# Performance work log

Hardware: AMD Instinct MI355X
Metric: run time of the kernel (lower is better)

## Reference

```python
import jax, jax.numpy as jnp
import numpy as np

HEAD_SIZE = 32


def setup_inputs() -> dict:
    key = jax.random.key(0)
    ks = jax.random.split(key, 9)
    B, N, M = 2, 512, 512
    Dq = Dk = Dv = 128
    De = 64
    H, O, OUT = 8, HEAD_SIZE, 128
    s = 0.05  # keep logits tame
    return {
        "query": jax.random.normal(ks[0], (B, N, Dq), jnp.float32),
        "key": jax.random.normal(ks[1], (B, M, Dk), jnp.float32),
        "value": jax.random.normal(ks[2], (B, M, Dv), jnp.float32),
        "edge": jax.random.normal(ks[3], (B, N, M, De), jnp.float32),
        "query_kernel": jax.random.normal(ks[4], (H, Dq, O), jnp.float32) * s,
        "key_kernel": jax.random.normal(ks[5], (H, Dk + De, O), jnp.float32) * s,
        "value_kernel": jax.random.normal(ks[6], (H, Dv, O), jnp.float32) * s,
        "projection_kernel": jax.random.normal(ks[7], (H, O, OUT), jnp.float32) * s,
        "projection_bias": jnp.zeros((OUT,), jnp.float32),
    }


def reference(query, key, value, edge, query_kernel, key_kernel,
              value_kernel, projection_kernel, projection_bias):
    # Edge-conditioned keys: concat broadcast key [B,1,M,Dk] with edge [B,N,M,De]
    B, N, _ = query.shape
    M = key.shape[-2]
    key_rep = jnp.broadcast_to(key[..., None, :, :], (B, N, M, key.shape[-1]))
    key_cat = jnp.concatenate([key_rep, edge], axis=-1)           # [B,N,M,Dk+De]
    k = jnp.einsum('bnmi,hio->bnmho', key_cat, key_kernel)        # [B,N,M,H,O]
    q = jnp.einsum('bni,hio->bnho', query, query_kernel)
    q = q / jnp.sqrt(jnp.asarray(HEAD_SIZE, q.dtype))
    v = jnp.einsum('bmi,hio->bmho', value, value_kernel)
    logits = jnp.einsum('bnho,bnmho->bhnm', q, k)                 # [B,H,N,M]
    attn = jax.nn.softmax(logits, axis=-1)
    mh = jnp.einsum('bhnm,bmho->bnho', attn, v)                   # [B,N,H,O]
    out = jnp.einsum('bnhi,hio->bno', mh, projection_kernel)
    out = out + projection_bias
    return out
```

## Files before the change

### kernel.cpp

```cpp
#include <hip/hip_runtime.h>

#define B_   2
#define N_   512
#define M_   512
#define D_   128
#define DE_  64
#define H_   8
#define O_   32
#define OUT_ 128
#define DKE_ 192
#define MP_  516

__global__ __launch_bounds__(256) void k_proj_a(
    const float* __restrict__ query, const float* __restrict__ Wq,
    const float* __restrict__ Wk, float* __restrict__ qE)
{
    const int r0 = blockIdx.x * 8;
    const int t  = threadIdx.x;
    __shared__ float Xs[8][D_];
    __shared__ float qh[8][H_ * O_];

    reinterpret_cast<float4*>(&Xs[0][0])[t] =
        reinterpret_cast<const float4*>(query + (size_t)r0 * D_)[t];
    __syncthreads();

    {
        float acc[8] = {0,0,0,0,0,0,0,0};
        const float* wcol = Wq + (t >> 5) * (D_ * O_) + (t & 31);
        for (int k = 0; k < D_; k += 4) {
            const float w0 = wcol[(k+0) * O_];
            const float w1 = wcol[(k+1) * O_];
            const float w2 = wcol[(k+2) * O_];
            const float w3 = wcol[(k+3) * O_];
#pragma unroll
            for (int r = 0; r < 8; ++r) {
                const float4 x = *reinterpret_cast<const float4*>(&Xs[r][k]);
                acc[r] += x.x * w0 + x.y * w1 + x.z * w2 + x.w * w3;
            }
        }
#pragma unroll
        for (int r = 0; r < 8; ++r) qh[r][t] = acc[r] * 0.17677669529663687f;
    }
    __syncthreads();

    for (int s = 0; s < 6; ++s) {
        const int hj = t + 256 * s;
        const int h  = hj / DKE_;
        float w[O_];
#pragma unroll
        for (int i = 0; i < O_ / 4; ++i) {
            const float4 x = reinterpret_cast<const float4*>(Wk + (size_t)hj * O_)[i];
            w[4*i] = x.x; w[4*i+1] = x.y; w[4*i+2] = x.z; w[4*i+3] = x.w;
        }
#pragma unroll
        for (int r = 0; r < 8; ++r) {
            const float* qrow = &qh[r][h * O_];
            float a = 0.f;
#pragma unroll
            for (int i = 0; i < O_ / 4; ++i) {
                const float4 qx = *reinterpret_cast<const float4*>(qrow + 4*i);
                a += qx.x * w[4*i] + qx.y * w[4*i+1] + qx.z * w[4*i+2] + qx.w * w[4*i+3];
            }
            qE[(size_t)(r0 + r) * (H_ * DKE_) + hj] = a;
        }
    }
}

__global__ __launch_bounds__(256) void k_proj_v(
    const float* __restrict__ value, const float* __restrict__ Wv,
    float* __restrict__ vo)
{
    const int r0 = blockIdx.x * 8;
    const int t  = threadIdx.x;
    __shared__ float Xs[8][D_];
    reinterpret_cast<float4*>(&Xs[0][0])[t] =
        reinterpret_cast<const float4*>(value + (size_t)r0 * D_)[t];
    __syncthreads();

    float acc[8] = {0,0,0,0,0,0,0,0};
    const float* wcol = Wv + (t >> 5) * (D_ * O_) + (t & 31);
    for (int k = 0; k < D_; k += 4) {
        const float w0 = wcol[(k+0) * O_];
        const float w1 = wcol[(k+1) * O_];
        const float w2 = wcol[(k+2) * O_];
        const float w3 = wcol[(k+3) * O_];
#pragma unroll
        for (int r = 0; r < 8; ++r) {
            const float4 x = *reinterpret_cast<const float4*>(&Xs[r][k]);
            acc[r] += x.x * w0 + x.y * w1 + x.z * w2 + x.w * w3;
        }
    }
#pragma unroll
    for (int r = 0; r < 8; ++r) vo[(size_t)(r0 + r) * (H_ * O_) + t] = acc[r];
}

__global__ __launch_bounds__(256) void k_attn(
    const float* __restrict__ key, const float* __restrict__ edge,
    const float* __restrict__ qE, const float* __restrict__ vv,
    const float* __restrict__ Wp, const float* __restrict__ bias,
    float* __restrict__ out)
{
    const int idx = blockIdx.x;
    const int b   = idx >> 9;
    const int t   = threadIdx.x;
    const int lane = t & 63;
    const int wv   = t >> 6;
    const int grp  = lane >> 4;
    const int el   = lane & 15;

    __shared__ float attn_s[H_][MP_];
    __shared__ float mh_s[H_ * O_];
    __shared__ float part_s[2][OUT_];

    float qf[8][12];
    {
        const float* base = qE + (size_t)idx * (H_ * DKE_);
#pragma unroll
        for (int h = 0; h < 8; ++h) {
#pragma unroll
            for (int p = 0; p < 3; ++p) {
                const float4 x = *reinterpret_cast<const float4*>(
                    base + h * DKE_ + p * 64 + el * 4);
                qf[h][4*p]   = x.x; qf[h][4*p+1] = x.y;
                qf[h][4*p+2] = x.z; qf[h][4*p+3] = x.w;
            }
        }
    }

    const float* keyb = key  + (size_t)b   * M_ * D_;
    const float* eb   = edge + (size_t)idx * M_ * DE_;
    const int sel3 = (el >> 3) & 1, sel2 = (el >> 2) & 1, sel1 = (el >> 1) & 1;

    for (int it = 0; it < 32; ++it) {
        const int m = it * 16 + wv * 4 + grp;
        const float4 k0 = *reinterpret_cast<const float4*>(keyb + (size_t)m * D_ + el * 4);
        const float4 k1 = *reinterpret_cast<const float4*>(keyb + (size_t)m * D_ + 64 + el * 4);
        const float4 e0 = *reinterpret_cast<const float4*>(eb + (size_t)m * DE_ + el * 4);
        float a[8];
#pragma unroll
        for (int h = 0; h < 8; ++h) {
            a[h] = qf[h][0]*k0.x + qf[h][1]*k0.y + qf[h][2]*k0.z + qf[h][3]*k0.w
                 + qf[h][4]*k1.x + qf[h][5]*k1.y + qf[h][6]*k1.z + qf[h][7]*k1.w
                 + qf[h][8]*e0.x + qf[h][9]*e0.y + qf[h][10]*e0.z + qf[h][11]*e0.w;
        }
        float b4[4];
#pragma unroll
        for (int q2 = 0; q2 < 4; ++q2) {
            const float tA = __shfl_xor(a[q2], 8, 16);
            const float tB = __shfl_xor(a[q2 + 4], 8, 16);
            b4[q2] = sel3 ? (a[q2 + 4] + tB) : (a[q2] + tA);
        }
        float c2[2];
#pragma unroll
        for (int q2 = 0; q2 < 2; ++q2) {
            const float tA = __shfl_xor(b4[q2], 4, 16);
            const float tB = __shfl_xor(b4[q2 + 2], 4, 16);
            c2[q2] = sel2 ? (b4[q2 + 2] + tB) : (b4[q2] + tA);
        }
        const float tA = __shfl_xor(c2[0], 2, 16);
        const float tB = __shfl_xor(c2[1], 2, 16);
        float d = sel1 ? (c2[1] + tB) : (c2[0] + tA);
        d += __shfl_xor(d, 1, 16);
        if ((el & 1) == 0) attn_s[(el >> 1) & 7][m] = d;
    }
    __syncthreads();

    {
        const int h = t >> 5, ml = t & 31;
        float mx = -3.4e38f;
#pragma unroll 2
        for (int j = 0; j < 16; ++j) mx = fmaxf(mx, attn_s[h][ml + 32 * j]);
#pragma unroll
        for (int mask = 16; mask >= 1; mask >>= 1) mx = fmaxf(mx, __shfl_xor(mx, mask, 64));
        float sum = 0.f;
#pragma unroll 2
        for (int j = 0; j < 16; ++j) {
            const int m = ml + 32 * j;
            const float p = __expf(attn_s[h][m] - mx);
            attn_s[h][m] = p;
            sum += p;
        }
#pragma unroll
        for (int mask = 16; mask >= 1; mask >>= 1) sum += __shfl_xor(sum, mask, 64);
        const float inv = 1.f / sum;
#pragma unroll 2
        for (int j = 0; j < 16; ++j) attn_s[h][ml + 32 * j] *= inv;
    }
    __syncthreads();

    {
        const int hh = t >> 5;
        const float* vb = vv + (size_t)b * M_ * (H_ * O_) + t;
        float a0 = 0.f, a1 = 0.f, a2 = 0.f, a3 = 0.f;
        for (int m = 0; m < M_; m += 4) {
            const float4 aw = *reinterpret_cast<const float4*>(&attn_s[hh][m]);
            a0 += aw.x * vb[(size_t)(m + 0) * 256];
            a1 += aw.y * vb[(size_t)(m + 1) * 256];
            a2 += aw.z * vb[(size_t)(m + 2) * 256];
            a3 += aw.w * vb[(size_t)(m + 3) * 256];
        }
        mh_s[t] = (a0 + a1) + (a2 + a3);
    }
    __syncthreads();

    {
        const int half = t >> 7;
        const int c = t & 127;
        float acc = 0.f;
        const int j0 = half * 128;
#pragma unroll 8
        for (int jj = 0; jj < 128; ++jj)
            acc += mh_s[j0 + jj] * Wp[(size_t)(j0 + jj) * OUT_ + c];
        part_s[half][c] = acc;
    }
    __syncthreads();
    if (t < OUT_)
        out[(size_t)idx * OUT_ + t] = part_s[0][t] + part_s[1][t] + bias[t];
}

extern "C" void kernel_launch(void* const* d_in, const int* in_sizes, int n_in,
                              void* d_out, int out_size, void* d_ws, size_t ws_size,
                              hipStream_t stream)
{
    const float* query = (const float*)d_in[0];
    const float* key   = (const float*)d_in[1];
    const float* value = (const float*)d_in[2];
    const float* edge  = (const float*)d_in[3];
    const float* Wq    = (const float*)d_in[4];
    const float* Wk    = (const float*)d_in[5];
    const float* Wv    = (const float*)d_in[6];
    const float* Wp    = (const float*)d_in[7];
    const float* bias  = (const float*)d_in[8];
    float* out = (float*)d_out;

    float* ws    = (float*)d_ws;
    float* qE_ws = ws;
    float* v_ws  = ws + (size_t)B_ * N_ * H_ * DKE_;

    k_proj_a<<<(B_ * N_) / 8, 256, 0, stream>>>(query, Wq, Wk, qE_ws);
    k_proj_v<<<(B_ * M_) / 8, 256, 0, stream>>>(value, Wv, v_ws);
    k_attn  <<<B_ * N_, 256, 0, stream>>>(key, edge, qE_ws, v_ws, Wp, bias, out);
}
```

Measured before the change: 297.0 us.

## Compute edge-conditioned logits with bf16 MFMA and register double-buffered key/edge loads

Replaces the scalar FMA plus shuffle-reduction logit computation with bf16 MFMA 16x16x32 instructions. The folded query-key projection is stored in bf16, and key/edge rows are converted to bf16 into a per-wave LDS tile. Key and edge loads are double-buffered in registers to overlap global traffic with compute, and launch bounds now request 3 blocks per CU. This trades logit precision (bf16 inputs) and wastes half the MFMA rows, since only 8 heads fill the 16-row tile. The kernel is likely bound by the 128 MB edge stream, so the gain may be limited.

```diff
diff --git a/kernel.cpp b/kernel.cpp
--- a/kernel.cpp
+++ b/kernel.cpp
@@ -1,4 +1,5 @@
 #include <hip/hip_runtime.h>
+#include <hip/hip_bf16.h>
 
 #define B_   2
 #define N_   512
@@ -10,10 +11,25 @@
 #define OUT_ 128
 #define DKE_ 192
 #define MP_  516
+#define BTP_ 200
+
+typedef unsigned short u16;
+typedef unsigned int   u32;
+typedef short bf16x8 __attribute__((ext_vector_type(8)));
+typedef float floatx4 __attribute__((ext_vector_type(4)));
+
+__device__ __forceinline__ u32 pk2bf(float a, float b) {
+    __hip_bfloat162 h = __float22bfloat162_rn(make_float2(a, b));
+    return *reinterpret_cast<u32*>(&h);
+}
+__device__ __forceinline__ u16 f2bf(float a) {
+    __hip_bfloat16 h = __float2bfloat16(a);
+    return *reinterpret_cast<u16*>(&h);
+}
 
 __global__ __launch_bounds__(256) void k_proj_a(
     const float* __restrict__ query, const float* __restrict__ Wq,
-    const float* __restrict__ Wk, float* __restrict__ qE)
+    const float* __restrict__ Wk, u16* __restrict__ qE)
 {
     const int r0 = blockIdx.x * 8;
     const int t  = threadIdx.x;
@@ -61,7 +77,7 @@
                 const float4 qx = *reinterpret_cast<const float4*>(qrow + 4*i);
                 a += qx.x * w[4*i] + qx.y * w[4*i+1] + qx.z * w[4*i+2] + qx.w * w[4*i+3];
             }
-            qE[(size_t)(r0 + r) * (H_ * DKE_) + hj] = a;
+            qE[(size_t)(r0 + r) * (H_ * DKE_) + hj] = f2bf(a);
         }
     }
 }
@@ -94,74 +110,98 @@
     for (int r = 0; r < 8; ++r) vo[(size_t)(r0 + r) * (H_ * O_) + t] = acc[r];
 }
 
-__global__ __launch_bounds__(256) void k_attn(
+__global__ __launch_bounds__(256, 3) void k_attn(
     const float* __restrict__ key, const float* __restrict__ edge,
-    const float* __restrict__ qE, const float* __restrict__ vv,
+    const u16* __restrict__ qE, const float* __restrict__ vv,
     const float* __restrict__ Wp, const float* __restrict__ bias,
     float* __restrict__ out)
 {
-    const int idx = blockIdx.x;
-    const int b   = idx >> 9;
-    const int t   = threadIdx.x;
+    const int idx  = blockIdx.x;
+    const int b    = idx >> 9;
+    const int t    = threadIdx.x;
     const int lane = t & 63;
     const int wv   = t >> 6;
-    const int grp  = lane >> 4;
-    const int el   = lane & 15;
-
-    __shared__ float attn_s[H_][MP_];
+
+    __shared__ __attribute__((aligned(16))) u16 Bt[4][16][BTP_];
+    __shared__ __attribute__((aligned(16))) float attn_s[H_][MP_];
     __shared__ float mh_s[H_ * O_];
     __shared__ float part_s[2][OUT_];
 
-    float qf[8][12];
-    {
-        const float* base = qE + (size_t)idx * (H_ * DKE_);
-#pragma unroll
-        for (int h = 0; h < 8; ++h) {
-#pragma unroll
-            for (int p = 0; p < 3; ++p) {
-                const float4 x = *reinterpret_cast<const float4*>(
-                    base + h * DKE_ + p * 64 + el * 4);
-                qf[h][4*p]   = x.x; qf[h][4*p+1] = x.y;
-                qf[h][4*p+2] = x.z; qf[h][4*p+3] = x.w;
-            }
+    bf16x8 afr[6];
+    {
+        const int ar = lane & 15, aq = lane >> 4;
+        if (ar < 8) {
+            const u16* ab = qE + (size_t)idx * (H_ * DKE_) + ar * DKE_;
+#pragma unroll
+            for (int kk = 0; kk < 6; ++kk)
+                afr[kk] = *reinterpret_cast<const bf16x8*>(ab + kk * 32 + aq * 8);
+        } else {
+#pragma unroll
+            for (int kk = 0; kk < 6; ++kk) afr[kk] = bf16x8{0,0,0,0,0,0,0,0};
         }
     }
 
     const float* keyb = key  + (size_t)b   * M_ * D_;
     const float* eb   = edge + (size_t)idx * M_ * DE_;
-    const int sel3 = (el >> 3) & 1, sel2 = (el >> 2) & 1, sel1 = (el >> 1) & 1;
-
-    for (int it = 0; it < 32; ++it) {
-        const int m = it * 16 + wv * 4 + grp;
-        const float4 k0 = *reinterpret_cast<const float4*>(keyb + (size_t)m * D_ + el * 4);
-        const float4 k1 = *reinterpret_cast<const float4*>(keyb + (size_t)m * D_ + 64 + el * 4);
-        const float4 e0 = *reinterpret_cast<const float4*>(eb + (size_t)m * DE_ + el * 4);
-        float a[8];
-#pragma unroll
-        for (int h = 0; h < 8; ++h) {
-            a[h] = qf[h][0]*k0.x + qf[h][1]*k0.y + qf[h][2]*k0.z + qf[h][3]*k0.w
-                 + qf[h][4]*k1.x + qf[h][5]*k1.y + qf[h][6]*k1.z + qf[h][7]*k1.w
-                 + qf[h][8]*e0.x + qf[h][9]*e0.y + qf[h][10]*e0.z + qf[h][11]*e0.w;
-        }
-        float b4[4];
-#pragma unroll
-        for (int q2 = 0; q2 < 4; ++q2) {
-            const float tA = __shfl_xor(a[q2], 8, 16);
-            const float tB = __shfl_xor(a[q2 + 4], 8, 16);
-            b4[q2] = sel3 ? (a[q2 + 4] + tB) : (a[q2] + tA);
-        }
-        float c2[2];
-#pragma unroll
-        for (int q2 = 0; q2 < 2; ++q2) {
-            const float tA = __shfl_xor(b4[q2], 4, 16);
-            const float tB = __shfl_xor(b4[q2 + 2], 4, 16);
-            c2[q2] = sel2 ? (b4[q2 + 2] + tB) : (b4[q2] + tA);
-        }
-        const float tA = __shfl_xor(c2[0], 2, 16);
-        const float tB = __shfl_xor(c2[1], 2, 16);
-        float d = sel1 ? (c2[1] + tB) : (c2[0] + tA);
-        d += __shfl_xor(d, 1, 16);
-        if ((el & 1) == 0) attn_s[(el >> 1) & 7][m] = d;
+    const int r  = lane >> 2;
+    const int s4 = lane & 3;
+
+    float4 kreg[2][8], ereg[2][4];
+
+    {
+        const int m0 = wv * 16;
+        const float* kr = keyb + (size_t)(m0 + r) * D_ + s4 * 32;
+        const float* er = eb   + (size_t)(m0 + r) * DE_ + s4 * 16;
+#pragma unroll
+        for (int i = 0; i < 8; ++i) kreg[0][i] = *reinterpret_cast<const float4*>(kr + i * 4);
+#pragma unroll
+        for (int i = 0; i < 4; ++i) ereg[0][i] = *reinterpret_cast<const float4*>(er + i * 4);
+    }
+
+    int buf = 0;
+    for (int it = 0; it < 8; ++it) {
+        const int tl = it * 4 + wv;
+        if (it < 7) {
+            const int m0 = (tl + 4) * 16;
+            const float* kr = keyb + (size_t)(m0 + r) * D_ + s4 * 32;
+            const float* er = eb   + (size_t)(m0 + r) * DE_ + s4 * 16;
+#pragma unroll
+            for (int i = 0; i < 8; ++i) kreg[buf^1][i] = *reinterpret_cast<const float4*>(kr + i * 4);
+#pragma unroll
+            for (int i = 0; i < 4; ++i) ereg[buf^1][i] = *reinterpret_cast<const float4*>(er + i * 4);
+        }
+        {
+            u16* dst = &Bt[wv][r][0];
+#pragma unroll
+            for (int i = 0; i < 8; ++i) {
+                uint2 p;
+                p.x = pk2bf(kreg[buf][i].x, kreg[buf][i].y);
+                p.y = pk2bf(kreg[buf][i].z, kreg[buf][i].w);
+                *reinterpret_cast<uint2*>(dst + s4 * 32 + i * 4) = p;
+            }
+#pragma unroll
+            for (int i = 0; i < 4; ++i) {
+                uint2 p;
+                p.x = pk2bf(ereg[buf][i].x, ereg[buf][i].y);
+                p.y = pk2bf(ereg[buf][i].z, ereg[buf][i].w);
+                *reinterpret_cast<uint2*>(dst + D_ + s4 * 16 + i * 4) = p;
+            }
+        }
+        {
+            const int br = lane & 15, q = lane >> 4;
+            floatx4 acc = {0.f, 0.f, 0.f, 0.f};
+#pragma unroll
+            for (int kk = 0; kk < 6; ++kk) {
+                const bf16x8 bfr = *reinterpret_cast<const bf16x8*>(&Bt[wv][br][kk * 32 + q * 8]);
+                acc = __builtin_amdgcn_mfma_f32_16x16x32_bf16(afr[kk], bfr, acc, 0, 0, 0);
+            }
+            if (q < 2) {
+#pragma unroll
+                for (int i = 0; i < 4; ++i)
+                    attn_s[q * 4 + i][tl * 16 + br] = acc[i];
+            }
+        }
+        buf ^= 1;
     }
     __syncthreads();
 
@@ -233,9 +273,8 @@
     const float* bias  = (const float*)d_in[8];
     float* out = (float*)d_out;
 
-    float* ws    = (float*)d_ws;
-    float* qE_ws = ws;
-    float* v_ws  = ws + (size_t)B_ * N_ * H_ * DKE_;
+    u16*   qE_ws = (u16*)d_ws;
+    float* v_ws  = (float*)((char*)d_ws + (size_t)B_*N_*H_*DKE_*2);
 
     k_proj_a<<<(B_ * N_) / 8, 256, 0, stream>>>(query, Wq, Wk, qE_ws);
     k_proj_v<<<(B_ * M_) / 8, 256, 0, stream>>>(value, Wv, v_ws);
```

After: 289.8 us. 2.4% less time.
